# Kernel optimization log

Hardware: AMD Instinct MI355X
Metric: run time of the kernel (lower is better)

The kernel has to match this reference:

```python
import jax, jax.numpy as jnp
import numpy as np

D_MODEL = 1024
D_FFN = 4096
NUM_EXPERTS = 8
TOP_K = 2
EPS = 1e-7


def setup_inputs() -> dict:
    key = jax.random.key(0)
    ks = jax.random.split(key, 10)
    B, T = 2, 2048
    s = 0.02
    return {
        "x": jax.random.normal(ks[0], (B, T, D_MODEL), dtype=jnp.float32),
        "padding_mask": jnp.ones((B, T), dtype=bool),
        "rms_w": jnp.ones((D_MODEL,), dtype=jnp.float32),
        "router_w": jax.random.normal(ks[1], (NUM_EXPERTS, D_MODEL), dtype=jnp.float32) * s,
        "router_b": jnp.zeros((NUM_EXPERTS,), dtype=jnp.float32),
        "W1": jax.random.normal(ks[2], (NUM_EXPERTS, D_MODEL, D_FFN), dtype=jnp.float32) * s,
        "b1": jnp.zeros((NUM_EXPERTS, D_FFN), dtype=jnp.float32),
        "W2": jax.random.normal(ks[3], (NUM_EXPERTS, D_FFN, D_MODEL), dtype=jnp.float32) * s,
        "b2": jnp.zeros((NUM_EXPERTS, D_MODEL), dtype=jnp.float32),
        "W3": jax.random.normal(ks[4], (NUM_EXPERTS, D_MODEL, D_FFN), dtype=jnp.float32) * s,
        "b3": jnp.zeros((NUM_EXPERTS, D_FFN), dtype=jnp.float32),
    }


def reference(x, padding_mask, rms_w, router_w, router_b, W1, b1, W2, b2, W3, b3):
    B, T, d = x.shape
    # RMSNorm
    rms = jnp.sqrt(jnp.mean(x * x, axis=-1, keepdims=True) + EPS)
    xn = rms_w * (x / rms)
    xf = xn.reshape(-1, d)  # [N, d]

    # Router: softmax -> top-k -> renormalize
    logits = xf @ router_w.T + router_b            # [N, E]
    probs = jax.nn.softmax(logits, axis=-1)
    topv, topi = jax.lax.top_k(probs, TOP_K)       # [N, K]
    w = topv / jnp.sum(topv, axis=-1, keepdims=True)
    # Dense combine weights per (token, expert): sum of top-k weights routed to e
    combine = jnp.sum(jax.nn.one_hot(topi, NUM_EXPERTS, dtype=xf.dtype) * w[..., None], axis=1)  # [N, E]

    # Loop over experts via scan (one full-token SwiGLU FFN per expert, masked combine)
    def step(acc, params):
        W1e, b1e, W2e, b2e, W3e, b3e, ce = params
        h = jax.nn.silu(xf @ W1e + b1e) * (xf @ W3e + b3e)  # [N, d_ffn]
        y = h @ W2e + b2e                                    # [N, d]
        return acc + ce[:, None] * y, None

    out, _ = jax.lax.scan(step, jnp.zeros_like(xf), (W1, b1, W2, b2, W3, b3, combine.T))
    aux_loss = jnp.asarray(0.0, dtype=x.dtype)  # use_aux_loss only active in training mode
    return out.reshape(B, T, d), aux_loss
```

## Files before the change

kernel.cpp:

```cpp
#include <hip/hip_runtime.h>
#include <stdint.h>


#define NTOK 4096
#define DM   1024
#define DF   4096
#define NE   8
#define BM   128
#define MAX_RB 72
#define SLOT_CAP (MAX_RB * BM)

typedef _Float16 f16;
typedef __attribute__((ext_vector_type(8))) _Float16 f16x8;
typedef __attribute__((ext_vector_type(4))) _Float16 f16x4;
typedef __attribute__((ext_vector_type(4))) float    f32x4;

__device__ __forceinline__ void gl2lds16(const void* g, void* l) {
  __builtin_amdgcn_global_load_lds(
      (const __attribute__((address_space(1))) unsigned int*)g,
      (__attribute__((address_space(3))) unsigned int*)l, 16, 0, 0);
}

__global__ __launch_bounds__(256) void k_rms_router(
    const float* __restrict__ x, const float* __restrict__ rms_w,
    const float* __restrict__ rw, const float* __restrict__ rbias,
    f16* __restrict__ xn, int* __restrict__ topi, float* __restrict__ topw,
    int* __restrict__ counts)
{
  int t = blockIdx.x;
  int tid = threadIdx.x;
  const float* xr = x + (size_t)t * DM;
  f32x4 xv = *(const f32x4*)(xr + tid * 4);
  f32x4 gw = *(const f32x4*)(rms_w + tid * 4);
  f32x4 gv = xv * gw;

  float v[9];
  v[8] = xv[0]*xv[0] + xv[1]*xv[1] + xv[2]*xv[2] + xv[3]*xv[3];
#pragma unroll
  for (int e = 0; e < NE; ++e) {
    f32x4 wv = *(const f32x4*)(rw + e * DM + tid * 4);
    v[e] = gv[0]*wv[0] + gv[1]*wv[1] + gv[2]*wv[2] + gv[3]*wv[3];
  }
#pragma unroll
  for (int off = 32; off; off >>= 1) {
#pragma unroll
    for (int j = 0; j < 9; ++j) v[j] += __shfl_xor(v[j], off);
  }
  __shared__ float red[4][9];
  int wave = tid >> 6, lane = tid & 63;
  if (lane == 0) {
#pragma unroll
    for (int j = 0; j < 9; ++j) red[wave][j] = v[j];
  }
  __syncthreads();
  float tot[9];
#pragma unroll
  for (int j = 0; j < 9; ++j)
    tot[j] = red[0][j] + red[1][j] + red[2][j] + red[3][j];

  float rinv = 1.0f / sqrtf(tot[8] * (1.0f / DM) + 1e-7f);
  float lg[NE];
#pragma unroll
  for (int e = 0; e < NE; ++e) lg[e] = tot[e] * rinv + rbias[e];

  int e1 = 0; float b1v = lg[0];
#pragma unroll
  for (int e = 1; e < NE; ++e) if (lg[e] > b1v) { b1v = lg[e]; e1 = e; }
  int e2 = -1; float b2v = -1e30f;
#pragma unroll
  for (int e = 0; e < NE; ++e) if (e != e1 && lg[e] > b2v) { b2v = lg[e]; e2 = e; }

  float r2 = expf(b2v - b1v);
  float w1 = 1.0f / (1.0f + r2);
  float w2 = r2 * w1;

  if (tid == 0) {
    topi[t * 2 + 0] = e1; topi[t * 2 + 1] = e2;
    topw[t * 2 + 0] = w1; topw[t * 2 + 1] = w2;
    atomicAdd(&counts[e1], 1);
    atomicAdd(&counts[e2], 1);
  }
  f16x4 o;
#pragma unroll
  for (int i = 0; i < 4; ++i) o[i] = (f16)(gv[i] * rinv);
  *(f16x4*)(xn + (size_t)t * DM + tid * 4) = o;
}

__global__ void k_build(const int* __restrict__ counts, int* __restrict__ po,
                        int2* __restrict__ rbtable, int* __restrict__ total_rb)
{
  if (threadIdx.x != 0 || blockIdx.x != 0) return;
  int off = 0, idx = 0;
  for (int e = 0; e < NE; ++e) {
    int c = counts[e];
    po[e] = off;
    int nrb = (c + BM - 1) / BM;
    for (int r = 0; r < nrb; ++r) { rbtable[idx] = make_int2(e, off + r * BM); ++idx; }
    off += nrb * BM;
  }
  *total_rb = idx;
}

__global__ __launch_bounds__(256) void k_assign(
    const int* __restrict__ topi, const float* __restrict__ topw,
    const int* __restrict__ po, int* __restrict__ cursors,
    int* __restrict__ slot_token, float* __restrict__ slot_w,
    int* __restrict__ tok2slot)
{
  int t = blockIdx.x * 256 + threadIdx.x;
  if (t >= NTOK) return;
#pragma unroll
  for (int k = 0; k < 2; ++k) {
    int e = topi[t * 2 + k];
    int pos = atomicAdd(&cursors[e], 1);
    int slot = po[e] + pos;
    slot_token[slot] = t;
    slot_w[slot] = topw[t * 2 + k];
    tok2slot[t * 2 + k] = slot;
  }
}

__global__ __launch_bounds__(256) void k_convw(
    const float* __restrict__ W1, const float* __restrict__ W3,
    f16* __restrict__ w16)
{
  __shared__ f16 T[64][132];
  int g = blockIdx.x;
  int tensor = g >> 12;
  int rem = g & 4095;
  int e = rem >> 9;
  int t = rem & 511;
  const float* W = (tensor == 0) ? W1 : W3;
  int np = t >> 4, kt = t & 15;
  const float* src = W + (size_t)e * DM * DF + (size_t)(kt * 64) * DF + np * 128;

  int tid = threadIdx.x;
  int q = tid & 31, kb = tid >> 5;
#pragma unroll
  for (int i = 0; i < 8; ++i) {
    int k = kb + 8 * i;
    f32x4 v = *(const f32x4*)(src + (size_t)k * DF + q * 4);
    f16x4 h4 = { (f16)v[0], (f16)v[1], (f16)v[2], (f16)v[3] };
    *(f16x4*)(&T[k][q * 4]) = h4;
  }
  __syncthreads();
  int n = tid >> 1;
  f16* dst = w16 + ((size_t)(tensor * NE + e) * 512 + t) * 8192 + n * 64 + (tid & 1) * 32;
#pragma unroll
  for (int qq = 0; qq < 4; ++qq) {
    int cs = (tid & 1) * 4 + qq;
    int cl = cs ^ (n & 7);
    f16x8 o;
#pragma unroll
    for (int j = 0; j < 8; ++j) o[j] = T[cl * 8 + j][n];
    *(f16x8*)(dst + qq * 8) = o;
  }
}

__global__ __launch_bounds__(256, 3) void k_ffn13(
    const f16* __restrict__ xn, const int* __restrict__ slot_token,
    const int2* __restrict__ rbtable, const int* __restrict__ total_rb,
    const f16* __restrict__ w16,
    const float* __restrict__ b1, const float* __restrict__ b3,
    const float* __restrict__ W2, f16* __restrict__ w16_w2,
    f16* __restrict__ h)
{
  __shared__ __align__(16) f16 As[128 * 64];
  __shared__ __align__(16) f16 Bs[2][128 * 64];

  int bid = blockIdx.x;
  int xcd = bid & 7, i = bid >> 3;
  int rbi = (i / 12) * 3 + (i % 3);
  int np  = xcd * 4 + ((i / 3) & 3);
  int tid = threadIdx.x, lane = tid & 63, wave = tid >> 6;

  bool active = (rbi < *total_rb);
  if (active) {
    int2 ent = rbtable[rbi];
    int e = ent.x, row0 = ent.y;
    int n0 = np * 128;

    int wm = wave >> 1, wn = wave & 1;
    const f16* wb1 = w16 + ((size_t)(0 * NE + e) * 512 + np * 16) * 8192;
    const f16* wb3 = w16 + ((size_t)(1 * NE + e) * 512 + np * 16) * 8192;

    int tok[4];
#pragma unroll
    for (int q = 0; q < 4; ++q) {
      int m = q * 32 + wave * 8 + (lane >> 3);
      int tkn = slot_token[row0 + m];
      tok[q] = (tkn < 0) ? 0 : tkn;
    }
    int csx = (((lane & 7) ^ (lane >> 3)) << 3);
    int lin = wave * 512 + lane * 8;

    f32x4 acc1[4][4], acc3[4][4];
    f32x4 z = {0.f, 0.f, 0.f, 0.f};
#pragma unroll
    for (int i2 = 0; i2 < 4; ++i2)
#pragma unroll
      for (int j = 0; j < 4; ++j) { acc1[i2][j] = z; acc3[i2][j] = z; }

    for (int kt = 0; kt < DM / 64; ++kt) {
      int k0 = kt * 64;
      const f16* s1 = wb1 + (size_t)kt * 8192;
      const f16* s3 = wb3 + (size_t)kt * 8192;
#pragma unroll
      for (int q = 0; q < 4; ++q) {
        gl2lds16(xn + (size_t)tok[q] * DM + k0 + csx,
                 (char*)As + q * 4096 + wave * 1024);
        gl2lds16(s1 + q * 2048 + lin, (char*)Bs[0] + q * 4096 + wave * 1024);
        gl2lds16(s3 + q * 2048 + lin, (char*)Bs[1] + q * 4096 + wave * 1024);
      }
      __syncthreads();
#pragma unroll
      for (int kh = 0; kh < 2; ++kh) {
        int kk = kh * 32 + (lane >> 4) * 8;
        f16x8 a[4];
#pragma unroll
        for (int fm = 0; fm < 4; ++fm) {
          int m = wm * 64 + fm * 16 + (lane & 15);
          a[fm] = *(const f16x8*)((char*)As + m * 128 + 2 * (kk ^ ((m & 7) << 3)));
        }
#pragma unroll
        for (int fn = 0; fn < 4; ++fn) {
          int n = wn * 64 + fn * 16 + (lane & 15);
          f16x8 bf1 = *(const f16x8*)((char*)Bs[0] + n * 128 + 2 * (kk ^ ((n & 7) << 3)));
          f16x8 bf3 = *(const f16x8*)((char*)Bs[1] + n * 128 + 2 * (kk ^ ((n & 7) << 3)));
#pragma unroll
          for (int fm = 0; fm < 4; ++fm) {
            acc1[fm][fn] = __builtin_amdgcn_mfma_f32_16x16x32_f16(a[fm], bf1, acc1[fm][fn], 0, 0, 0);
            acc3[fm][fn] = __builtin_amdgcn_mfma_f32_16x16x32_f16(a[fm], bf3, acc3[fm][fn], 0, 0, 0);
          }
        }
      }
      __syncthreads();
    }
#pragma unroll
    for (int fn = 0; fn < 4; ++fn) {
      int nc = n0 + wn * 64 + fn * 16 + (lane & 15);
      float bb1 = b1[e * DF + nc], bb3 = b3[e * DF + nc];
#pragma unroll
      for (int fm = 0; fm < 4; ++fm) {
        int mbase = wm * 64 + fm * 16 + (lane >> 4) * 4;
#pragma unroll
        for (int r = 0; r < 4; ++r) {
          int sl = mbase + r;
          float u1 = acc1[fm][fn][r] + bb1;
          float u3 = acc3[fm][fn][r] + bb3;
          float hv = (u1 / (1.0f + __expf(-u1))) * u3;
          size_t off = (size_t)(row0 + sl) * DF + (nc & ~63)
                     + ((((nc >> 3) & 7) ^ (sl & 7)) << 3) + (nc & 7);
          h[off] = (f16)hv;
        }
      }
    }
  }

  f16 (*T)[132] = (f16(*)[132])(&Bs[0][0]);
  int q = tid & 31, kb = tid >> 5;
  for (int j = 0; j < 2; ++j) {
    int tile = bid * 2 + j;
    if (tile >= NE * 512) break;
    int e2 = tile >> 9, t2 = tile & 511;
    int np2 = t2 >> 6, kt2 = t2 & 63;
    const float* src = W2 + (size_t)e2 * DM * DF + (size_t)(kt2 * 64) * DM + np2 * 128;
    __syncthreads();
#pragma unroll
    for (int i2 = 0; i2 < 8; ++i2) {
      int k = kb + 8 * i2;
      f32x4 v = *(const f32x4*)(src + (size_t)k * DM + q * 4);
      f16x4 h4 = { (f16)v[0], (f16)v[1], (f16)v[2], (f16)v[3] };
      *(f16x4*)(&T[k][q * 4]) = h4;
    }
    __syncthreads();
    int n = tid >> 1;
    f16* dst = w16_w2 + (size_t)(e2 * 512 + t2) * 8192 + n * 64 + (tid & 1) * 32;
#pragma unroll
    for (int qq = 0; qq < 4; ++qq) {
      int cs = (tid & 1) * 4 + qq;
      int cl = cs ^ (n & 7);
      f16x8 o8;
#pragma unroll
      for (int jj = 0; jj < 8; ++jj) o8[jj] = T[cl * 8 + jj][n];
      *(f16x8*)(dst + qq * 8) = o8;
    }
  }
}

__global__ __launch_bounds__(256, 4) void k_ffn2(
    const f16* __restrict__ h,
    const int2* __restrict__ rbtable, const int* __restrict__ total_rb,
    const f16* __restrict__ w16_w2, f16* __restrict__ partial)
{
  int bid = blockIdx.x;
  int xcd = bid & 7, i = bid >> 3;
  int rbi_in  = i % 3;
  int np      = (i / 3) & 7;
  int kc      = (i / 24) & 3;
  int rbi_out = i / 96;
  int rbi = xcd + 8 * (rbi_out * 3 + rbi_in);
  if (rbi >= *total_rb) return;
  int2 ent = rbtable[rbi];
  int e = ent.x, row0 = ent.y;
  int n0 = np * 128;

  __shared__ __align__(16) f16 As[128 * 64];
  __shared__ __align__(16) f16 Bsh[128 * 64];

  int tid = threadIdx.x, lane = tid & 63, wave = tid >> 6;
  int wm = wave >> 1, wn = wave & 1;
  const f16* wb = w16_w2 + ((size_t)e * 512 + np * 64 + kc * 16) * 8192;
  int lin = wave * 512 + lane * 8;

  f32x4 acc[4][4];
  f32x4 z = {0.f, 0.f, 0.f, 0.f};
#pragma unroll
  for (int i2 = 0; i2 < 4; ++i2)
#pragma unroll
    for (int j = 0; j < 4; ++j) acc[i2][j] = z;

  for (int kt = 0; kt < 16; ++kt) {
    const f16* sB = wb + (size_t)kt * 8192;
    int k0 = kc * 1024 + kt * 64;
#pragma unroll
    for (int q = 0; q < 4; ++q) {
      int m = q * 32 + wave * 8 + (lane >> 3);
      gl2lds16(h + (size_t)(row0 + m) * DF + k0 + ((lane & 7) << 3),
               (char*)As + q * 4096 + wave * 1024);
      gl2lds16(sB + q * 2048 + lin, (char*)Bsh + q * 4096 + wave * 1024);
    }
    __syncthreads();
#pragma unroll
    for (int kh = 0; kh < 2; ++kh) {
      int kk = kh * 32 + (lane >> 4) * 8;
      f16x8 a[4];
#pragma unroll
      for (int fm = 0; fm < 4; ++fm) {
        int m = wm * 64 + fm * 16 + (lane & 15);
        a[fm] = *(const f16x8*)((char*)As + m * 128 + 2 * (kk ^ ((m & 7) << 3)));
      }
#pragma unroll
      for (int fn = 0; fn < 4; ++fn) {
        int n = wn * 64 + fn * 16 + (lane & 15);
        f16x8 bf = *(const f16x8*)((char*)Bsh + n * 128 + 2 * (kk ^ ((n & 7) << 3)));
#pragma unroll
        for (int fm = 0; fm < 4; ++fm)
          acc[fm][fn] = __builtin_amdgcn_mfma_f32_16x16x32_f16(a[fm], bf, acc[fm][fn], 0, 0, 0);
      }
    }
    __syncthreads();
  }
#pragma unroll
  for (int fn = 0; fn < 4; ++fn) {
    int nc = n0 + wn * 64 + fn * 16 + (lane & 15);
#pragma unroll
    for (int fm = 0; fm < 4; ++fm) {
      int mbase = wm * 64 + fm * 16 + (lane >> 4) * 4;
#pragma unroll
      for (int r = 0; r < 4; ++r) {
        int slot = row0 + mbase + r;
        partial[((size_t)(kc * SLOT_CAP + slot) << 10) + nc] = (f16)acc[fm][fn][r];
      }
    }
  }
}

__global__ __launch_bounds__(256) void k_combine(
    const f16* __restrict__ partial, const int* __restrict__ tok2slot,
    const int* __restrict__ topi, const float* __restrict__ topw,
    const float* __restrict__ b2, float* __restrict__ out)
{
  int t = blockIdx.x;
  int nc = threadIdx.x * 4;
  int s1 = tok2slot[t * 2], s2 = tok2slot[t * 2 + 1];
  float c1 = topw[t * 2], c2 = topw[t * 2 + 1];
  int e1 = topi[t * 2], e2 = topi[t * 2 + 1];
  float y1[4] = {0.f, 0.f, 0.f, 0.f}, y2[4] = {0.f, 0.f, 0.f, 0.f};
#pragma unroll
  for (int kc = 0; kc < 4; ++kc) {
    f16x4 p1 = *(const f16x4*)(partial + (((size_t)(kc * SLOT_CAP + s1)) << 10) + nc);
    f16x4 p2 = *(const f16x4*)(partial + (((size_t)(kc * SLOT_CAP + s2)) << 10) + nc);
#pragma unroll
    for (int i = 0; i < 4; ++i) { y1[i] += (float)p1[i]; y2[i] += (float)p2[i]; }
  }
  f32x4 bb1 = *(const f32x4*)(b2 + e1 * DM + nc);
  f32x4 bb2 = *(const f32x4*)(b2 + e2 * DM + nc);
  f32x4 o;
#pragma unroll
  for (int i = 0; i < 4; ++i)
    o[i] = c1 * (y1[i] + bb1[i]) + c2 * (y2[i] + bb2[i]);
  *(f32x4*)(out + ((size_t)t << 10) + nc) = o;
}

extern "C" void kernel_launch(void* const* d_in, const int* in_sizes, int n_in,
                              void* d_out, int out_size, void* d_ws, size_t ws_size,
                              hipStream_t stream)
{
  const float* x     = (const float*)d_in[0];
  const float* rms_w = (const float*)d_in[2];
  const float* rw    = (const float*)d_in[3];
  const float* rbias = (const float*)d_in[4];
  const float* W1    = (const float*)d_in[5];
  const float* b1    = (const float*)d_in[6];
  const float* W2    = (const float*)d_in[7];
  const float* b2    = (const float*)d_in[8];
  const float* W3    = (const float*)d_in[9];
  const float* b3    = (const float*)d_in[10];
  float* out = (float*)d_out;

  char* ws = (char*)d_ws;
  size_t o = 0;
  f16* w16 = (f16*)(ws + o); o += (size_t)3 * NE * 512 * 8192 * 2;
  f16* h   = (f16*)(ws + o); o += (size_t)SLOT_CAP * DF * 2;
  f16* xn  = (f16*)(ws + o); o += (size_t)NTOK * DM * 2;
  int*   slot_token = (int*)(ws + o);   o += SLOT_CAP * 4;
  float* slot_w     = (float*)(ws + o); o += SLOT_CAP * 4;
  int*   topi       = (int*)(ws + o);   o += NTOK * 2 * 4;
  float* topw       = (float*)(ws + o); o += NTOK * 2 * 4;
  int*   tok2slot   = (int*)(ws + o);   o += NTOK * 2 * 4;
  int*   counts     = (int*)(ws + o);   o += 64;
  int*   cursors    = (int*)(ws + o);   o += 64;
  int*   po         = (int*)(ws + o);   o += 64;
  int*   total_rb   = (int*)(ws + o);   o += 64;
  int2*  rbtable    = (int2*)(ws + o);  o += MAX_RB * 8;
  (void)ws_size; (void)in_sizes; (void)n_in;

  f16* w16_w2 = w16 + (size_t)2 * NE * 512 * 8192;
  f16* partial = w16;

  hipMemsetAsync(d_out, 0, (size_t)out_size * 4, stream);
  hipMemsetAsync(counts, 0, 128, stream);
  hipMemsetAsync(slot_token, 0xFF, SLOT_CAP * 4, stream);

  k_convw<<<2 * NE * 512, 256, 0, stream>>>(W1, W3, w16);
  k_rms_router<<<NTOK, 256, 0, stream>>>(x, rms_w, rw, rbias, xn, topi, topw, counts);
  k_build<<<1, 64, 0, stream>>>(counts, po, rbtable, total_rb);
  k_assign<<<16, 256, 0, stream>>>(topi, topw, po, cursors, slot_token, slot_w, tok2slot);
  k_ffn13<<<8 * 288, 256, 0, stream>>>(xn, slot_token, rbtable, total_rb,
                                       w16, b1, b3, W2, w16_w2, h);
  k_ffn2<<<8 * 288, 256, 0, stream>>>(h, rbtable, total_rb, w16_w2, partial);
  k_combine<<<NTOK, 256, 0, stream>>>(partial, tok2slot, topi, topw, b2, out);
}
```

Baseline: 525.6 us.

## Widen FFN2 tile to 128x256 and halve split-K to two chunks

Each k_ffn2 block now computes two 128-column panes, sharing one A tile of h across both, and covers twice the K range (2048 instead of 1024). That cuts the grid from 2304 to 576 blocks and leaves two partial buffers for k_combine to sum instead of four. The aim is less redundant loading of h, less fp16 partial-sum write/read traffic, and fewer blocks to schedule. In exchange it doubles the accumulator registers and adds LDS, lowering occupancy to 3 blocks per CU, and it gives fewer blocks for load balancing across CUs.

```diff
diff --git a/kernel.cpp b/kernel.cpp
--- a/kernel.cpp
+++ b/kernel.cpp
@@ -288,47 +288,49 @@
   }
 }
 
-__global__ __launch_bounds__(256, 4) void k_ffn2(
+__global__ __launch_bounds__(256, 3) void k_ffn2(
     const f16* __restrict__ h,
     const int2* __restrict__ rbtable, const int* __restrict__ total_rb,
     const f16* __restrict__ w16_w2, f16* __restrict__ partial)
 {
+  __shared__ __align__(16) f16 As[128 * 64];
+  __shared__ __align__(16) f16 Bsh[2][128 * 64];
+
   int bid = blockIdx.x;
   int xcd = bid & 7, i = bid >> 3;
   int rbi_in  = i % 3;
-  int np      = (i / 3) & 7;
-  int kc      = (i / 24) & 3;
-  int rbi_out = i / 96;
+  int npp     = (i / 3) & 3;
+  int kc      = (i / 12) & 1;
+  int rbi_out = i / 24;
   int rbi = xcd + 8 * (rbi_out * 3 + rbi_in);
   if (rbi >= *total_rb) return;
   int2 ent = rbtable[rbi];
   int e = ent.x, row0 = ent.y;
-  int n0 = np * 128;
-
-  __shared__ __align__(16) f16 As[128 * 64];
-  __shared__ __align__(16) f16 Bsh[128 * 64];
 
   int tid = threadIdx.x, lane = tid & 63, wave = tid >> 6;
   int wm = wave >> 1, wn = wave & 1;
-  const f16* wb = w16_w2 + ((size_t)e * 512 + np * 64 + kc * 16) * 8192;
+  const f16* wb0 = w16_w2 + ((size_t)e * 512 + (npp * 2) * 64 + kc * 32) * 8192;
+  const f16* wb1 = wb0 + (size_t)64 * 8192;
   int lin = wave * 512 + lane * 8;
 
-  f32x4 acc[4][4];
+  f32x4 acc0[4][4], acc1[4][4];
   f32x4 z = {0.f, 0.f, 0.f, 0.f};
 #pragma unroll
   for (int i2 = 0; i2 < 4; ++i2)
 #pragma unroll
-    for (int j = 0; j < 4; ++j) acc[i2][j] = z;
-
-  for (int kt = 0; kt < 16; ++kt) {
-    const f16* sB = wb + (size_t)kt * 8192;
-    int k0 = kc * 1024 + kt * 64;
+    for (int j = 0; j < 4; ++j) { acc0[i2][j] = z; acc1[i2][j] = z; }
+
+  for (int kt = 0; kt < 32; ++kt) {
+    const f16* s0 = wb0 + (size_t)kt * 8192;
+    const f16* s1 = wb1 + (size_t)kt * 8192;
+    int k0 = kc * 2048 + kt * 64;
 #pragma unroll
     for (int q = 0; q < 4; ++q) {
       int m = q * 32 + wave * 8 + (lane >> 3);
       gl2lds16(h + (size_t)(row0 + m) * DF + k0 + ((lane & 7) << 3),
                (char*)As + q * 4096 + wave * 1024);
-      gl2lds16(sB + q * 2048 + lin, (char*)Bsh + q * 4096 + wave * 1024);
+      gl2lds16(s0 + q * 2048 + lin, (char*)Bsh[0] + q * 4096 + wave * 1024);
+      gl2lds16(s1 + q * 2048 + lin, (char*)Bsh[1] + q * 4096 + wave * 1024);
     }
     __syncthreads();
 #pragma unroll
@@ -343,24 +345,31 @@
 #pragma unroll
       for (int fn = 0; fn < 4; ++fn) {
         int n = wn * 64 + fn * 16 + (lane & 15);
-        f16x8 bf = *(const f16x8*)((char*)Bsh + n * 128 + 2 * (kk ^ ((n & 7) << 3)));
-#pragma unroll
-        for (int fm = 0; fm < 4; ++fm)
-          acc[fm][fn] = __builtin_amdgcn_mfma_f32_16x16x32_f16(a[fm], bf, acc[fm][fn], 0, 0, 0);
+        f16x8 bf0 = *(const f16x8*)((char*)Bsh[0] + n * 128 + 2 * (kk ^ ((n & 7) << 3)));
+        f16x8 bf1 = *(const f16x8*)((char*)Bsh[1] + n * 128 + 2 * (kk ^ ((n & 7) << 3)));
+#pragma unroll
+        for (int fm = 0; fm < 4; ++fm) {
+          acc0[fm][fn] = __builtin_amdgcn_mfma_f32_16x16x32_f16(a[fm], bf0, acc0[fm][fn], 0, 0, 0);
+          acc1[fm][fn] = __builtin_amdgcn_mfma_f32_16x16x32_f16(a[fm], bf1, acc1[fm][fn], 0, 0, 0);
+        }
       }
     }
     __syncthreads();
   }
 #pragma unroll
-  for (int fn = 0; fn < 4; ++fn) {
-    int nc = n0 + wn * 64 + fn * 16 + (lane & 15);
-#pragma unroll
-    for (int fm = 0; fm < 4; ++fm) {
-      int mbase = wm * 64 + fm * 16 + (lane >> 4) * 4;
-#pragma unroll
-      for (int r = 0; r < 4; ++r) {
-        int slot = row0 + mbase + r;
-        partial[((size_t)(kc * SLOT_CAP + slot) << 10) + nc] = (f16)acc[fm][fn][r];
+  for (int pane = 0; pane < 2; ++pane) {
+#pragma unroll
+    for (int fn = 0; fn < 4; ++fn) {
+      int nc = npp * 256 + pane * 128 + wn * 64 + fn * 16 + (lane & 15);
+#pragma unroll
+      for (int fm = 0; fm < 4; ++fm) {
+        int mbase = wm * 64 + fm * 16 + (lane >> 4) * 4;
+#pragma unroll
+        for (int r = 0; r < 4; ++r) {
+          int slot = row0 + mbase + r;
+          float vv = pane ? acc1[fm][fn][r] : acc0[fm][fn][r];
+          partial[((size_t)(kc * SLOT_CAP + slot) << 10) + nc] = (f16)vv;
+        }
       }
     }
   }
@@ -378,7 +387,7 @@
   int e1 = topi[t * 2], e2 = topi[t * 2 + 1];
   float y1[4] = {0.f, 0.f, 0.f, 0.f}, y2[4] = {0.f, 0.f, 0.f, 0.f};
 #pragma unroll
-  for (int kc = 0; kc < 4; ++kc) {
+  for (int kc = 0; kc < 2; ++kc) {
     f16x4 p1 = *(const f16x4*)(partial + (((size_t)(kc * SLOT_CAP + s1)) << 10) + nc);
     f16x4 p2 = *(const f16x4*)(partial + (((size_t)(kc * SLOT_CAP + s2)) << 10) + nc);
 #pragma unroll
@@ -439,6 +448,6 @@
   k_assign<<<16, 256, 0, stream>>>(topi, topw, po, cursors, slot_token, slot_w, tok2slot);
   k_ffn13<<<8 * 288, 256, 0, stream>>>(xn, slot_token, rbtable, total_rb,
                                        w16, b1, b3, W2, w16_w2, h);
-  k_ffn2<<<8 * 288, 256, 0, stream>>>(h, rbtable, total_rb, w16_w2, partial);
+  k_ffn2<<<8 * 72, 256, 0, stream>>>(h, rbtable, total_rb, w16_w2, partial);
   k_combine<<<NTOK, 256, 0, stream>>>(partial, tok2slot, topi, topw, b2, out);
 }
```

New measurement: 520.9 us. About the same (-0.9%).

## Fuse combine into FFN2 epilogue with atomic scatter and drop split-K

Applied to the files above, without the earlier changes.

Removes the split-K partial buffer and the separate combine kernel: each FFN2 block now iterates the full 4096-wide K dimension and scatters its weighted, bias-added outputs directly into the fp32 output with atomicAdd. This avoids writing and rereading the fp16 partial tensor and one kernel launch. The trade-off is a quarter as many blocks (576 vs 2304), which lowers parallelism, plus scattered float atomics to out. Precision also changes slightly since partial sums are no longer rounded to fp16.

```diff
diff --git a/kernel.cpp b/kernel.cpp
--- a/kernel.cpp
+++ b/kernel.cpp
@@ -104,8 +104,7 @@
 __global__ __launch_bounds__(256) void k_assign(
     const int* __restrict__ topi, const float* __restrict__ topw,
     const int* __restrict__ po, int* __restrict__ cursors,
-    int* __restrict__ slot_token, float* __restrict__ slot_w,
-    int* __restrict__ tok2slot)
+    int* __restrict__ slot_token, float* __restrict__ slot_w)
 {
   int t = blockIdx.x * 256 + threadIdx.x;
   if (t >= NTOK) return;
@@ -116,7 +115,6 @@
     int slot = po[e] + pos;
     slot_token[slot] = t;
     slot_w[slot] = topw[t * 2 + k];
-    tok2slot[t * 2 + k] = slot;
   }
 }
 
@@ -289,28 +287,29 @@
 }
 
 __global__ __launch_bounds__(256, 4) void k_ffn2(
-    const f16* __restrict__ h,
+    const f16* __restrict__ h, const int* __restrict__ slot_token,
+    const float* __restrict__ slot_w,
     const int2* __restrict__ rbtable, const int* __restrict__ total_rb,
-    const f16* __restrict__ w16_w2, f16* __restrict__ partial)
-{
+    const f16* __restrict__ w16_w2, const float* __restrict__ b2,
+    float* __restrict__ out)
+{
+  __shared__ __align__(16) f16 As[128 * 64];
+  __shared__ __align__(16) f16 Bsh[128 * 64];
+
   int bid = blockIdx.x;
   int xcd = bid & 7, i = bid >> 3;
   int rbi_in  = i % 3;
-  int np      = (i / 3) & 7;
-  int kc      = (i / 24) & 3;
-  int rbi_out = i / 96;
+  int np      = (i / 3) % 8;
+  int rbi_out = i / 24;
   int rbi = xcd + 8 * (rbi_out * 3 + rbi_in);
   if (rbi >= *total_rb) return;
   int2 ent = rbtable[rbi];
   int e = ent.x, row0 = ent.y;
   int n0 = np * 128;
 
-  __shared__ __align__(16) f16 As[128 * 64];
-  __shared__ __align__(16) f16 Bsh[128 * 64];
-
   int tid = threadIdx.x, lane = tid & 63, wave = tid >> 6;
   int wm = wave >> 1, wn = wave & 1;
-  const f16* wb = w16_w2 + ((size_t)e * 512 + np * 64 + kc * 16) * 8192;
+  const f16* wb = w16_w2 + ((size_t)e * 512 + np * 64) * 8192;
   int lin = wave * 512 + lane * 8;
 
   f32x4 acc[4][4];
@@ -320,9 +319,9 @@
 #pragma unroll
     for (int j = 0; j < 4; ++j) acc[i2][j] = z;
 
-  for (int kt = 0; kt < 16; ++kt) {
+  for (int kt = 0; kt < 64; ++kt) {
     const f16* sB = wb + (size_t)kt * 8192;
-    int k0 = kc * 1024 + kt * 64;
+    int k0 = kt * 64;
 #pragma unroll
     for (int q = 0; q < 4; ++q) {
       int m = q * 32 + wave * 8 + (lane >> 3);
@@ -351,46 +350,30 @@
     }
     __syncthreads();
   }
+  int   tk[4][4];
+  float cw[4][4];
+#pragma unroll
+  for (int fm = 0; fm < 4; ++fm) {
+#pragma unroll
+    for (int r = 0; r < 4; ++r) {
+      int slot = row0 + wm * 64 + fm * 16 + (lane >> 4) * 4 + r;
+      tk[fm][r] = slot_token[slot];
+      cw[fm][r] = slot_w[slot];
+    }
+  }
 #pragma unroll
   for (int fn = 0; fn < 4; ++fn) {
     int nc = n0 + wn * 64 + fn * 16 + (lane & 15);
+    float bb = b2[e * DM + nc];
 #pragma unroll
     for (int fm = 0; fm < 4; ++fm) {
-      int mbase = wm * 64 + fm * 16 + (lane >> 4) * 4;
 #pragma unroll
       for (int r = 0; r < 4; ++r) {
-        int slot = row0 + mbase + r;
-        partial[((size_t)(kc * SLOT_CAP + slot) << 10) + nc] = (f16)acc[fm][fn][r];
-      }
-    }
-  }
-}
-
-__global__ __launch_bounds__(256) void k_combine(
-    const f16* __restrict__ partial, const int* __restrict__ tok2slot,
-    const int* __restrict__ topi, const float* __restrict__ topw,
-    const float* __restrict__ b2, float* __restrict__ out)
-{
-  int t = blockIdx.x;
-  int nc = threadIdx.x * 4;
-  int s1 = tok2slot[t * 2], s2 = tok2slot[t * 2 + 1];
-  float c1 = topw[t * 2], c2 = topw[t * 2 + 1];
-  int e1 = topi[t * 2], e2 = topi[t * 2 + 1];
-  float y1[4] = {0.f, 0.f, 0.f, 0.f}, y2[4] = {0.f, 0.f, 0.f, 0.f};
-#pragma unroll
-  for (int kc = 0; kc < 4; ++kc) {
-    f16x4 p1 = *(const f16x4*)(partial + (((size_t)(kc * SLOT_CAP + s1)) << 10) + nc);
-    f16x4 p2 = *(const f16x4*)(partial + (((size_t)(kc * SLOT_CAP + s2)) << 10) + nc);
-#pragma unroll
-    for (int i = 0; i < 4; ++i) { y1[i] += (float)p1[i]; y2[i] += (float)p2[i]; }
-  }
-  f32x4 bb1 = *(const f32x4*)(b2 + e1 * DM + nc);
-  f32x4 bb2 = *(const f32x4*)(b2 + e2 * DM + nc);
-  f32x4 o;
-#pragma unroll
-  for (int i = 0; i < 4; ++i)
-    o[i] = c1 * (y1[i] + bb1[i]) + c2 * (y2[i] + bb2[i]);
-  *(f32x4*)(out + ((size_t)t << 10) + nc) = o;
+        if (tk[fm][r] >= 0)
+          atomicAdd(out + (size_t)tk[fm][r] * DM + nc, cw[fm][r] * (acc[fm][fn][r] + bb));
+      }
+    }
+  }
 }
 
 extern "C" void kernel_launch(void* const* d_in, const int* in_sizes, int n_in,
@@ -418,7 +401,6 @@
   float* slot_w     = (float*)(ws + o); o += SLOT_CAP * 4;
   int*   topi       = (int*)(ws + o);   o += NTOK * 2 * 4;
   float* topw       = (float*)(ws + o); o += NTOK * 2 * 4;
-  int*   tok2slot   = (int*)(ws + o);   o += NTOK * 2 * 4;
   int*   counts     = (int*)(ws + o);   o += 64;
   int*   cursors    = (int*)(ws + o);   o += 64;
   int*   po         = (int*)(ws + o);   o += 64;
@@ -427,7 +409,6 @@
   (void)ws_size; (void)in_sizes; (void)n_in;
 
   f16* w16_w2 = w16 + (size_t)2 * NE * 512 * 8192;
-  f16* partial = w16;
 
   hipMemsetAsync(d_out, 0, (size_t)out_size * 4, stream);
   hipMemsetAsync(counts, 0, 128, stream);
@@ -436,9 +417,9 @@
   k_convw<<<2 * NE * 512, 256, 0, stream>>>(W1, W3, w16);
   k_rms_router<<<NTOK, 256, 0, stream>>>(x, rms_w, rw, rbias, xn, topi, topw, counts);
   k_build<<<1, 64, 0, stream>>>(counts, po, rbtable, total_rb);
-  k_assign<<<16, 256, 0, stream>>>(topi, topw, po, cursors, slot_token, slot_w, tok2slot);
+  k_assign<<<16, 256, 0, stream>>>(topi, topw, po, cursors, slot_token, slot_w);
   k_ffn13<<<8 * 288, 256, 0, stream>>>(xn, slot_token, rbtable, total_rb,
                                        w16, b1, b3, W2, w16_w2, h);
-  k_ffn2<<<8 * 288, 256, 0, stream>>>(h, rbtable, total_rb, w16_w2, partial);
-  k_combine<<<NTOK, 256, 0, stream>>>(partial, tok2slot, topi, topw, b2, out);
-}
+  k_ffn2<<<8 * 72, 256, 0, stream>>>(h, slot_token, slot_w, rbtable, total_rb,
+                                     w16_w2, b2, out);
+}
```

Result: slower. 539.5 us (+2.7%).
